# Optimization experiments

Measured on AMD Instinct MI355X. Metric: run time of the kernel, lower is better.

Reference implementation:

```python
import jax, jax.numpy as jnp
import numpy as np

S_LEN, T_LEN, BATCH, HID = 32, 32, 64, 512


def setup_inputs() -> dict:
    key = jax.random.key(0)
    ks = jax.random.split(key, 5)
    H = HID
    sc = lambda n: 1.0 / np.sqrt(n)
    return {
        "source": jax.random.normal(ks[0], (S_LEN, BATCH, H), jnp.float32),
        "target": jax.random.normal(ks[1], (T_LEN, BATCH, H), jnp.float32),
        # H2h Dense: concat(s_h, t_h) [B, 2H] -> [B, H], linear
        "W_H2h": (jax.random.normal(ks[2], (2 * H, H), jnp.float32) * sc(2 * H)),
        "b_H2h": jnp.zeros((H,), jnp.float32),
        # shared LSTMCell weights (Keras gate order i, f, g, o)
        "W_kernel": (jax.random.normal(ks[3], (H, 4 * H), jnp.float32) * sc(H)),
        "W_rec": (jax.random.normal(ks[4], (H, 4 * H), jnp.float32) * sc(H)),
        "b_lstm": jnp.zeros((4 * H,), jnp.float32),
    }


def _lstm_cell(x, h, c, Wk, Wr, b):
    # Keras LSTMCell math, gate order i, f, g(candidate), o
    z = x @ Wk + h @ Wr + b  # [B, 4H]
    i, f, g, o = jnp.split(z, 4, axis=-1)
    c2 = jax.nn.sigmoid(f) * c + jax.nn.sigmoid(i) * jnp.tanh(g)
    h2 = jax.nn.sigmoid(o) * jnp.tanh(c2)
    return h2, c2


def reference(source, target, W_H2h, b_H2h, W_kernel, W_rec, b_lstm):
    # source: [S, B, H] (time-major), target: [T, B, H]
    T, B, H = target.shape

    def inner(s_state, t_slice):
        # s_state carried along the target axis; t_slice is target cell j state
        s_step, s_h, s_m = s_state
        t_step, t_h, t_m = t_slice
        hmid = jnp.concatenate([s_h, t_h], axis=1) @ W_H2h + b_H2h  # [B, H]
        ns_h, ns_m = _lstm_cell(s_step, hmid, s_m, W_kernel, W_rec, b_lstm)
        nt_h, nt_m = _lstm_cell(t_step, hmid, t_m, W_kernel, W_rec, b_lstm)
        # step arrays get overwritten with the new hidden state
        return (ns_h, ns_h, ns_m), (nt_h, nt_h, nt_m)

    def outer(t_arrays, s_in):
        # fresh source state per outer step i: step = source[i], h = m = 0
        z = jnp.zeros_like(s_in)
        (s_step_f, _, _), t_new = jax.lax.scan(inner, (s_in, z, z), t_arrays)
        return t_new, s_step_f

    zeros = jnp.zeros((T, B, H), source.dtype)
    t_final, source_out = jax.lax.scan(outer, (target, zeros, zeros), source)
    return source_out, t_final[0]
```

## Files before the change

### kernel.cpp

```cpp
#include <hip/hip_runtime.h>

#define BLK 256

typedef __bf16 bf16;
typedef __bf16 bf16x8 __attribute__((ext_vector_type(8)));
typedef float f32x4 __attribute__((ext_vector_type(4)));

__device__ __forceinline__ float sigm(float x) { return 1.f / (1.f + __expf(-x)); }
__device__ __forceinline__ float tanh_(float x) {
    x = fminf(fmaxf(x, -15.f), 15.f);
    float e = __expf(2.f * x);
    return (e - 1.f) / (e + 1.f);
}

__device__ __forceinline__ void gl2lds(const bf16* g, bf16* l) {
    __builtin_amdgcn_global_load_lds((const __attribute__((address_space(1))) void*)g,
                                     (__attribute__((address_space(3))) void*)l, 16, 0, 0);
}


__global__ void k_cast(const float* __restrict__ in, bf16* __restrict__ out, int n) {
    int i = blockIdx.x * BLK + threadIdx.x;
    if (i < n) out[i] = (bf16)in[i];
}

__global__ void k_cast2(const float* __restrict__ in, bf16* __restrict__ hi,
                        bf16* __restrict__ lo, int n) {
    int i = blockIdx.x * BLK + threadIdx.x;
    if (i < n) {
        float v = in[i];
        bf16 h = (bf16)v;
        hi[i] = h;
        lo[i] = (bf16)(v - (float)h);
    }
}

__global__ void k_tcast2(const float* __restrict__ in, bf16* __restrict__ hi,
                         bf16* __restrict__ lo, int C) {
    int id = blockIdx.x * BLK + threadIdx.x;
    int c = id >> 9, r = id & 511;
    float v = in[(size_t)r * C + c];
    bf16 h = (bf16)v;
    hi[id] = h;
    if (lo) lo[id] = (bf16)(v - (float)h);
}

__global__ void k_bz(const float* __restrict__ bh, const float* __restrict__ Wr,
                     const float* __restrict__ bl, float* __restrict__ bz) {
    int c = blockIdx.x * BLK + threadIdx.x;
    float s = bl[c];
    for (int k = 0; k < 512; k++) s += bh[k] * Wr[(size_t)k * 2048 + c];
    bz[c] = s;
}

__global__ __launch_bounds__(256, 2) void k_gemmP(
    const bf16* __restrict__ Ahi, const bf16* __restrict__ Alo,
    const bf16* __restrict__ Bhi, const bf16* __restrict__ Blo,
    const float* __restrict__ Wk,
    bf16* __restrict__ P1, bf16* __restrict__ P3,
    bf16* __restrict__ P4, bf16* __restrict__ P5) {
    __shared__ __align__(16) bf16 At[64 * 72];
    __shared__ __align__(16) bf16 Bt[4 * 64 * 72];
    const int t = threadIdx.x, w = t >> 6, l = t & 63;
    const int m0 = (blockIdx.x >> 2) * 64, n0 = (blockIdx.x & 3) * 256;
    f32x4 acc[4][4] = {};
    const bf16* Aps[3] = {Ahi, Alo, Ahi};
    const bf16* Bps[3] = {Bhi, Bhi, Blo};
    for (int p = 0; p < 3; p++) {
        const bf16* Ap = Aps[p] + (size_t)m0 * 512;
        const bf16* Bp = Bps[p];
        for (int kt = 0; kt < 8; kt++) {
            int k0 = kt * 64;
            __syncthreads();
#pragma unroll
            for (int q = 0; q < 2; q++) {
                int idx = q * 256 + t, row = idx >> 3, cc = idx & 7;
                uint4 v = *(const uint4*)(Ap + (size_t)row * 512 + k0 + cc * 8);
                *(uint4*)&At[row * 72 + cc * 8] = v;
            }
#pragma unroll
            for (int q = 0; q < 8; q++) {
                int idx = q * 256 + t, g = idx >> 9, rr = (idx >> 3) & 63, cc = idx & 7;
                uint4 v = *(const uint4*)(Bp + (size_t)(n0 + g * 64 + rr) * 512 + k0 + cc * 8);
                *(uint4*)&Bt[(g * 64 + rr) * 72 + cc * 8] = v;
            }
            __syncthreads();
#pragma unroll
            for (int ks = 0; ks < 2; ks++) {
                int ko = ks * 32 + (l >> 4) * 8;
                bf16x8 af[4], bb[4];
#pragma unroll
                for (int mt = 0; mt < 4; mt++)
                    af[mt] = *(const bf16x8*)&At[(mt * 16 + (l & 15)) * 72 + ko];
#pragma unroll
                for (int g = 0; g < 4; g++)
                    bb[g] = *(const bf16x8*)&Bt[(g * 64 + w * 16 + (l & 15)) * 72 + ko];
#pragma unroll
                for (int mt = 0; mt < 4; mt++)
#pragma unroll
                    for (int g = 0; g < 4; g++)
                        acc[mt][g] = __builtin_amdgcn_mfma_f32_16x16x32_bf16(
                            af[mt], bb[g], acc[mt][g], 0, 0, 0);
            }
        }
    }
    const bool hihalf = (n0 >= 512);
#pragma unroll
    for (int mt = 0; mt < 4; mt++) {
#pragma unroll
        for (int g = 0; g < 4; g++) {
            int np = n0 + g * 64 + w * 16 + (l & 15);
#pragma unroll
            for (int r = 0; r < 4; r++) {
                int c = m0 + mt * 16 + ((l >> 4) << 2) + r;
                float v = acc[mt][g][r];
                if (!hihalf) {
                    P4[(size_t)c * 512 + np] = (bf16)v;
                    P1[(size_t)c * 512 + np] = (bf16)(v + Wk[(size_t)np * 2048 + c]);
                } else {
                    int kk = np - 512;
                    P3[(size_t)c * 512 + kk] = (bf16)v;
                    P5[(size_t)c * 512 + kk] = (bf16)(v + Wk[(size_t)kk * 2048 + c]);
                }
            }
        }
    }
}

__global__ __launch_bounds__(256, 4) void k_diag(
    int d, int i_lo,
    const bf16* __restrict__ srcb, const bf16* __restrict__ tgtb,
    const bf16* __restrict__ P1, const bf16* __restrict__ P2,
    const bf16* __restrict__ P3, const bf16* __restrict__ P4,
    const bf16* __restrict__ P5,
    const float* __restrict__ bz,
    const bf16* __restrict__ shR, bf16* __restrict__ shW,
    const bf16* __restrict__ thR, bf16* __restrict__ thW,
    float* __restrict__ sc, float* __restrict__ tc,
    float* __restrict__ out) {
    __shared__ __align__(16) bf16 At[64 * 64];
    __shared__ __align__(16) bf16 Bt[128 * 64];
    const int t = threadIdx.x, w = t >> 6, l = t & 63;
    const int cell = blockIdx.x >> 5, sub = blockIdx.x & 31;
    const int side = sub >> 4, ch0 = (sub & 15) << 5;
    const int i = i_lo + cell, j = d - i;
    const size_t stI = (size_t)i * 64 * 512, stJ = (size_t)j * 64 * 512;

    const bf16* Ah[2];
    const bf16* Wh[2];
    int nh = 0;
    if (side == 0) {
        Ah[nh] = (j == 0 ? srcb : shR) + stI;
        Wh[nh] = (j == 0 ? P2 : P1);
        nh++;
        if (i > 0) { Ah[nh] = thR + stJ; Wh[nh] = P3; nh++; }
    } else {
        if (j > 0) { Ah[nh] = shR + stI; Wh[nh] = P4; nh++; }
        Ah[nh] = (i == 0 ? tgtb : thR) + stJ;
        Wh[nh] = (i == 0 ? P2 : P5);
        nh++;
    }

    f32x4 acc[2][4] = {};
    for (int hh = 0; hh < nh; hh++) {
        const bf16* Ap = Ah[hh];
        const bf16* Wp = Wh[hh];
        for (int kt = 0; kt < 8; kt++) {
            int k0 = kt * 64;
            __syncthreads();
#pragma unroll
            for (int q = 0; q < 2; q++) {
                int p = q * 256 + t;
                int r = p >> 3, c = (p & 7) ^ (r & 7);
                gl2lds(Ap + (size_t)r * 512 + k0 + c * 8, &At[(q * 256 + w * 64) * 8]);
            }
#pragma unroll
            for (int q = 0; q < 4; q++) {
                int p = q * 256 + t;
                int r = p >> 3, c = (p & 7) ^ (r & 7);
                int g = r >> 5;
                gl2lds(Wp + (size_t)(g * 512 + ch0 + (r & 31)) * 512 + k0 + c * 8,
                       &Bt[(q * 256 + w * 64) * 8]);
            }
            __syncthreads();
#pragma unroll
            for (int ks = 0; ks < 2; ks++) {
                int c = ks * 4 + (l >> 4);
                bf16x8 af[2], bb[4];
#pragma unroll
                for (int mt = 0; mt < 2; mt++) {
                    int r = (w >> 1) * 32 + mt * 16 + (l & 15);
                    af[mt] = *(const bf16x8*)&At[(r * 8 + (c ^ (r & 7))) * 8];
                }
#pragma unroll
                for (int g = 0; g < 4; g++) {
                    int r = g * 32 + (w & 1) * 16 + (l & 15);
                    bb[g] = *(const bf16x8*)&Bt[(r * 8 + (c ^ (r & 7))) * 8];
                }
#pragma unroll
                for (int mt = 0; mt < 2; mt++)
#pragma unroll
                    for (int g = 0; g < 4; g++)
                        acc[mt][g] = __builtin_amdgcn_mfma_f32_16x16x32_bf16(
                            af[mt], bb[g], acc[mt][g], 0, 0, 0);
            }
        }
    }

    const int h = ch0 + (w & 1) * 16 + (l & 15);
    float bzv[4];
#pragma unroll
    for (int g = 0; g < 4; g++) bzv[g] = bz[g * 512 + h];
#pragma unroll
    for (int mt = 0; mt < 2; mt++) {
#pragma unroll
        for (int r = 0; r < 4; r++) {
            int b = (w >> 1) * 32 + mt * 16 + ((l >> 4) << 2) + r;
            float zi = acc[mt][0][r] + bzv[0];
            float zf = acc[mt][1][r] + bzv[1];
            float zg = acc[mt][2][r] + bzv[2];
            float zo = acc[mt][3][r] + bzv[3];
            if (side == 0) {
                size_t off = stI + (size_t)b * 512 + h;
                float cold = (j == 0) ? 0.f : sc[off];
                float c2 = sigm(zf) * cold + sigm(zi) * tanh_(zg);
                float h2 = sigm(zo) * tanh_(c2);
                sc[off] = c2;
                shW[off] = (bf16)h2;
                if (j == 31) out[off] = h2;
            } else {
                size_t off = stJ + (size_t)b * 512 + h;
                float cold = (i == 0) ? 0.f : tc[off];
                float c2 = sigm(zf) * cold + sigm(zi) * tanh_(zg);
                float h2 = sigm(zo) * tanh_(c2);
                tc[off] = c2;
                thW[off] = (bf16)h2;
                if (i == 31) out[1048576 + off] = h2;
            }
        }
    }
}


extern "C" void kernel_launch(void* const* d_in, const int* in_sizes, int n_in,
                              void* d_out, int out_size, void* d_ws, size_t ws_size,
                              hipStream_t stream) {
    const float* src = (const float*)d_in[0];
    const float* tgt = (const float*)d_in[1];
    const float* WH = (const float*)d_in[2];
    const float* bH = (const float*)d_in[3];
    const float* Wk = (const float*)d_in[4];
    const float* Wr = (const float*)d_in[5];
    const float* bl = (const float*)d_in[6];
    float* out = (float*)d_out;
    char* w = (char*)d_ws;
    const size_t MB = 1u << 20;
    bf16* srcb = (bf16*)(w + 0 * MB);
    bf16* tgtb = (bf16*)(w + 2 * MB);
    bf16* WHhi = (bf16*)(w + 4 * MB);
    bf16* WHlo = (bf16*)(w + 5 * MB);
    bf16* Wrhi = (bf16*)(w + 6 * MB);
    bf16* Wrlo = (bf16*)(w + 8 * MB);
    bf16* P1 = (bf16*)(w + 10 * MB);
    bf16* P2 = (bf16*)(w + 12 * MB);
    bf16* P3 = (bf16*)(w + 14 * MB);
    bf16* P4 = (bf16*)(w + 16 * MB);
    bf16* P5 = (bf16*)(w + 18 * MB);
    float* bz = (float*)(w + 20 * MB);
    bf16* sh = (bf16*)(w + 21 * MB);
    bf16* th = (bf16*)(w + 25 * MB);
    float* sc = (float*)(w + 29 * MB);
    float* tc = (float*)(w + 33 * MB);

    k_cast<<<4096, BLK, 0, stream>>>(src, srcb, 1048576);
    k_cast<<<4096, BLK, 0, stream>>>(tgt, tgtb, 1048576);
    k_cast2<<<2048, BLK, 0, stream>>>(WH, WHhi, WHlo, 524288);
    k_tcast2<<<4096, BLK, 0, stream>>>(Wr, Wrhi, Wrlo, 2048);
    k_tcast2<<<4096, BLK, 0, stream>>>(Wk, P2, nullptr, 2048);
    k_bz<<<8, BLK, 0, stream>>>(bH, Wr, bl, bz);
    k_gemmP<<<128, BLK, 0, stream>>>(Wrhi, Wrlo, WHhi, WHlo, Wk, P1, P3, P4, P5);

    for (int d = 0; d < 63; d++) {
        int i_lo = d > 31 ? d - 31 : 0;
        int i_hi = d < 31 ? d : 31;
        int Kd = i_hi - i_lo + 1;
        const bf16* shR = sh + (size_t)(d & 1) * 1048576;
        bf16* shW = sh + (size_t)((d + 1) & 1) * 1048576;
        const bf16* thR = th + (size_t)(d & 1) * 1048576;
        bf16* thW = th + (size_t)((d + 1) & 1) * 1048576;
        k_diag<<<Kd * 32, BLK, 0, stream>>>(d, i_lo, srcb, tgtb, P1, P2, P3, P4, P5,
                                            bz, shR, shW, thR, thW, sc, tc, out);
    }
}
```

Before: 1.467 ms.

## Replace per-diagonal launches with persistent wavefront kernel using per-cell dependency counters

Replaces the 63 per-diagonal kernel launches with a single persistent cooperative kernel. Blocks walk the tiles diagonal by diagonal and spin on per-cell completion counters in global memory before starting a cell. The five prep kernels are merged into one grid-stride kernel, which also zeroes the counters. The A operand is now read straight into registers with relaxed atomic loads instead of through LDS, each wave covers 16 rows and all 128 gate columns, and hidden states are written as packed pairs. This removes launch overhead and the full-grid barrier at each diagonal, at the cost of spin-wait latency and relaxed-ordering memory-visibility risks.

```diff
diff --git a/kernel.cpp b/kernel.cpp
--- a/kernel.cpp
+++ b/kernel.cpp
@@ -5,6 +5,7 @@
 typedef __bf16 bf16;
 typedef __bf16 bf16x8 __attribute__((ext_vector_type(8)));
 typedef float f32x4 __attribute__((ext_vector_type(4)));
+typedef unsigned long long u64;
 
 __device__ __forceinline__ float sigm(float x) { return 1.f / (1.f + __expf(-x)); }
 __device__ __forceinline__ float tanh_(float x) {
@@ -18,39 +19,47 @@
                                      (__attribute__((address_space(3))) void*)l, 16, 0, 0);
 }
 
-
-__global__ void k_cast(const float* __restrict__ in, bf16* __restrict__ out, int n) {
-    int i = blockIdx.x * BLK + threadIdx.x;
-    if (i < n) out[i] = (bf16)in[i];
-}
-
-__global__ void k_cast2(const float* __restrict__ in, bf16* __restrict__ hi,
-                        bf16* __restrict__ lo, int n) {
-    int i = blockIdx.x * BLK + threadIdx.x;
-    if (i < n) {
-        float v = in[i];
+#define ALOAD64(p) __hip_atomic_load((const u64*)(p), __ATOMIC_RELAXED, __HIP_MEMORY_SCOPE_AGENT)
+#define ALOADF(p) __hip_atomic_load((const float*)(p), __ATOMIC_RELAXED, __HIP_MEMORY_SCOPE_AGENT)
+#define ASTOREF(p, v) __hip_atomic_store((float*)(p), (v), __ATOMIC_RELAXED, __HIP_MEMORY_SCOPE_AGENT)
+#define ASTOREU(p, v) __hip_atomic_store((unsigned int*)(p), (v), __ATOMIC_RELAXED, __HIP_MEMORY_SCOPE_AGENT)
+
+__global__ void k_prep(const float* __restrict__ src, const float* __restrict__ tgt,
+                       const float* __restrict__ WH, const float* __restrict__ bH,
+                       const float* __restrict__ Wk, const float* __restrict__ Wr,
+                       const float* __restrict__ bl,
+                       bf16* __restrict__ srcb, bf16* __restrict__ tgtb,
+                       bf16* __restrict__ WHhi, bf16* __restrict__ WHlo,
+                       bf16* __restrict__ Wrhi, bf16* __restrict__ Wrlo,
+                       bf16* __restrict__ P2, float* __restrict__ bz,
+                       int* __restrict__ cellDone) {
+    const int gtid = blockIdx.x * BLK + threadIdx.x;
+    const int NT = gridDim.x * BLK;
+    for (int id = gtid; id < 1048576; id += NT) srcb[id] = (bf16)src[id];
+    for (int id = gtid; id < 1048576; id += NT) tgtb[id] = (bf16)tgt[id];
+    for (int id = gtid; id < 524288; id += NT) {
+        float v = WH[id];
         bf16 h = (bf16)v;
-        hi[i] = h;
-        lo[i] = (bf16)(v - (float)h);
-    }
-}
-
-__global__ void k_tcast2(const float* __restrict__ in, bf16* __restrict__ hi,
-                         bf16* __restrict__ lo, int C) {
-    int id = blockIdx.x * BLK + threadIdx.x;
-    int c = id >> 9, r = id & 511;
-    float v = in[(size_t)r * C + c];
-    bf16 h = (bf16)v;
-    hi[id] = h;
-    if (lo) lo[id] = (bf16)(v - (float)h);
-}
-
-__global__ void k_bz(const float* __restrict__ bh, const float* __restrict__ Wr,
-                     const float* __restrict__ bl, float* __restrict__ bz) {
-    int c = blockIdx.x * BLK + threadIdx.x;
-    float s = bl[c];
-    for (int k = 0; k < 512; k++) s += bh[k] * Wr[(size_t)k * 2048 + c];
-    bz[c] = s;
+        WHhi[id] = h;
+        WHlo[id] = (bf16)(v - (float)h);
+    }
+    for (int id = gtid; id < 1048576; id += NT) {
+        int c = id >> 9, r = id & 511;
+        float v = Wr[(size_t)r * 2048 + c];
+        bf16 h = (bf16)v;
+        Wrhi[id] = h;
+        Wrlo[id] = (bf16)(v - (float)h);
+    }
+    for (int id = gtid; id < 1048576; id += NT) {
+        int c = id >> 9, r = id & 511;
+        P2[id] = (bf16)Wk[(size_t)r * 2048 + c];
+    }
+    for (int id = gtid; id < 2048; id += NT) {
+        float s = bl[id];
+        for (int k = 0; k < 512; k++) s += bH[k] * Wr[(size_t)k * 2048 + id];
+        bz[id] = s;
+    }
+    for (int id = gtid; id < 1024; id += NT) cellDone[id] = 0;
 }
 
 __global__ __launch_bounds__(256, 2) void k_gemmP(
@@ -127,117 +136,161 @@
     }
 }
 
-__global__ __launch_bounds__(256, 4) void k_diag(
-    int d, int i_lo,
-    const bf16* __restrict__ srcb, const bf16* __restrict__ tgtb,
-    const bf16* __restrict__ P1, const bf16* __restrict__ P2,
-    const bf16* __restrict__ P3, const bf16* __restrict__ P4,
-    const bf16* __restrict__ P5,
-    const float* __restrict__ bz,
-    const bf16* __restrict__ shR, bf16* __restrict__ shW,
-    const bf16* __restrict__ thR, bf16* __restrict__ thW,
-    float* __restrict__ sc, float* __restrict__ tc,
-    float* __restrict__ out) {
-    __shared__ __align__(16) bf16 At[64 * 64];
+struct WaveP {
+    const bf16 *srcb, *tgtb, *P1, *P2, *P3, *P4, *P5;
+    const float* bz;
+    bf16 *sh, *th;
+    float *sc, *tc;
+    float* out;
+    int* cellDone;
+    int nblk;
+};
+
+__global__ __launch_bounds__(256, 4) void k_wave(WaveP p) {
     __shared__ __align__(16) bf16 Bt[128 * 64];
     const int t = threadIdx.x, w = t >> 6, l = t & 63;
-    const int cell = blockIdx.x >> 5, sub = blockIdx.x & 31;
-    const int side = sub >> 4, ch0 = (sub & 15) << 5;
-    const int i = i_lo + cell, j = d - i;
-    const size_t stI = (size_t)i * 64 * 512, stJ = (size_t)j * 64 * 512;
-
-    const bf16* Ah[2];
-    const bf16* Wh[2];
-    int nh = 0;
-    if (side == 0) {
-        Ah[nh] = (j == 0 ? srcb : shR) + stI;
-        Wh[nh] = (j == 0 ? P2 : P1);
-        nh++;
-        if (i > 0) { Ah[nh] = thR + stJ; Wh[nh] = P3; nh++; }
-    } else {
-        if (j > 0) { Ah[nh] = shR + stI; Wh[nh] = P4; nh++; }
-        Ah[nh] = (i == 0 ? tgtb : thR) + stJ;
-        Wh[nh] = (i == 0 ? P2 : P5);
-        nh++;
-    }
-
-    f32x4 acc[2][4] = {};
-    for (int hh = 0; hh < nh; hh++) {
-        const bf16* Ap = Ah[hh];
-        const bf16* Wp = Wh[hh];
-        for (int kt = 0; kt < 8; kt++) {
-            int k0 = kt * 64;
+    const int bid = blockIdx.x;
+    const int nblk = p.nblk;
+
+    int J = bid, base = 0;
+#pragma unroll 1
+    for (int d = 0; d < 63; d++) {
+        const int i_lo = d > 31 ? d - 31 : 0;
+        const int Kd = d < 32 ? d + 1 : 63 - d;
+        const int cnt = Kd * 32;
+#pragma unroll 1
+        while (J - base < cnt) {
+            const int tile = J - base;
+            const int cell = tile >> 5, sub = tile & 31;
+            const int side = sub >> 4, ch0 = (sub & 15) << 5;
+            const int i = i_lo + cell, j = d - i;
+            const size_t stI = (size_t)i * 64 * 512, stJ = (size_t)j * 64 * 512;
+
+            if (t == 0) {
+                if (j > 0)
+                    while (__hip_atomic_load(&p.cellDone[i * 32 + j - 1], __ATOMIC_RELAXED,
+                                             __HIP_MEMORY_SCOPE_AGENT) < 32)
+                        __builtin_amdgcn_s_sleep(4);
+                if (i > 0)
+                    while (__hip_atomic_load(&p.cellDone[(i - 1) * 32 + j], __ATOMIC_RELAXED,
+                                             __HIP_MEMORY_SCOPE_AGENT) < 32)
+                        __builtin_amdgcn_s_sleep(4);
+            }
             __syncthreads();
-#pragma unroll
-            for (int q = 0; q < 2; q++) {
-                int p = q * 256 + t;
-                int r = p >> 3, c = (p & 7) ^ (r & 7);
-                gl2lds(Ap + (size_t)r * 512 + k0 + c * 8, &At[(q * 256 + w * 64) * 8]);
-            }
-#pragma unroll
-            for (int q = 0; q < 4; q++) {
-                int p = q * 256 + t;
-                int r = p >> 3, c = (p & 7) ^ (r & 7);
-                int g = r >> 5;
-                gl2lds(Wp + (size_t)(g * 512 + ch0 + (r & 31)) * 512 + k0 + c * 8,
-                       &Bt[(q * 256 + w * 64) * 8]);
-            }
+
+            const bf16* shR = p.sh + (size_t)(d & 1) * 1048576;
+            bf16* shW = p.sh + (size_t)((d + 1) & 1) * 1048576;
+            const bf16* thR = p.th + (size_t)(d & 1) * 1048576;
+            bf16* thW = p.th + (size_t)((d + 1) & 1) * 1048576;
+
+            const bf16* Ah[2];
+            const bf16* Wh[2];
+            int nh = 0;
+            if (side == 0) {
+                Ah[nh] = (j == 0 ? p.srcb : shR) + stI;
+                Wh[nh] = (j == 0 ? p.P2 : p.P1);
+                nh++;
+                if (i > 0) { Ah[nh] = thR + stJ; Wh[nh] = p.P3; nh++; }
+            } else {
+                if (j > 0) { Ah[nh] = shR + stI; Wh[nh] = p.P4; nh++; }
+                Ah[nh] = (i == 0 ? p.tgtb : thR) + stJ;
+                Wh[nh] = (i == 0 ? p.P2 : p.P5);
+                nh++;
+            }
+
+            f32x4 acc[8] = {};
+            for (int hh = 0; hh < nh; hh++) {
+                const bf16* Ap = Ah[hh];
+                const bf16* Wp = Wh[hh];
+                for (int kt = 0; kt < 8; kt++) {
+                    int k0 = kt * 64;
+                    __syncthreads();
+#pragma unroll
+                    for (int q = 0; q < 4; q++) {
+                        int pp = q * 256 + t;
+                        int r = pp >> 3, c = (pp & 7) ^ (r & 7);
+                        int g = r >> 5;
+                        gl2lds(Wp + (size_t)(g * 512 + ch0 + (r & 31)) * 512 + k0 + c * 8,
+                               &Bt[(q * 256 + w * 64) * 8]);
+                    }
+                    u64 areg[2][2];
+                    {
+                        const int r = w * 16 + (l & 15);
+                        const u64* Ap64 = (const u64*)Ap + (size_t)r * 128;
+#pragma unroll
+                        for (int ks = 0; ks < 2; ks++) {
+                            int ko = k0 + ks * 32 + (l >> 4) * 8;
+                            areg[ks][0] = ALOAD64(Ap64 + (ko >> 2));
+                            areg[ks][1] = ALOAD64(Ap64 + (ko >> 2) + 1);
+                        }
+                    }
+                    __syncthreads();
+#pragma unroll
+                    for (int ks = 0; ks < 2; ks++) {
+                        int c = ks * 4 + (l >> 4);
+                        union { u64 u[2]; bf16x8 v; } cv;
+                        cv.u[0] = areg[ks][0];
+                        cv.u[1] = areg[ks][1];
+                        bf16x8 af = cv.v;
+#pragma unroll
+                        for (int g8 = 0; g8 < 8; g8++) {
+                            int r = g8 * 16 + (l & 15);
+                            bf16x8 bb = *(const bf16x8*)&Bt[(r * 8 + (c ^ (r & 7))) * 8];
+                            acc[g8] = __builtin_amdgcn_mfma_f32_16x16x32_bf16(af, bb, acc[g8], 0, 0, 0);
+                        }
+                    }
+                }
+            }
+
+            union { bf16 b; unsigned short s; } c0, c1;
+#pragma unroll
+            for (int hh16 = 0; hh16 < 2; hh16++) {
+                const int h = ch0 + hh16 * 16 + (l & 15);
+                float bzv[4];
+#pragma unroll
+                for (int g = 0; g < 4; g++) bzv[g] = p.bz[g * 512 + h];
+#pragma unroll
+                for (int r = 0; r < 4; r++) {
+                    int b = w * 16 + ((l >> 4) << 2) + r;
+                    float zi = acc[0 * 2 + hh16][r] + bzv[0];
+                    float zf = acc[1 * 2 + hh16][r] + bzv[1];
+                    float zg = acc[2 * 2 + hh16][r] + bzv[2];
+                    float zo = acc[3 * 2 + hh16][r] + bzv[3];
+                    size_t off = (side == 0 ? stI : stJ) + (size_t)b * 512 + h;
+                    float cold;
+                    if (side == 0)
+                        cold = (j == 0) ? 0.f : ALOADF(&p.sc[off]);
+                    else
+                        cold = (i == 0) ? 0.f : ALOADF(&p.tc[off]);
+                    float c2 = sigm(zf) * cold + sigm(zi) * tanh_(zg);
+                    float h2 = sigm(zo) * tanh_(c2);
+                    if (side == 0)
+                        ASTOREF(&p.sc[off], c2);
+                    else
+                        ASTOREF(&p.tc[off], c2);
+                    float hp = __shfl_xor(h2, 1);
+                    c0.b = (bf16)h2;
+                    c1.b = (bf16)hp;
+                    unsigned int packed = (unsigned int)c0.s | ((unsigned int)c1.s << 16);
+                    if (!(l & 1)) {
+                        bf16* hw = (side == 0 ? shW : thW);
+                        ASTOREU(&hw[off], packed);
+                    }
+                    if (side == 0) {
+                        if (j == 31) p.out[off] = h2;
+                    } else if (i == 31) {
+                        p.out[1048576 + off] = h2;
+                    }
+                }
+            }
+
             __syncthreads();
-#pragma unroll
-            for (int ks = 0; ks < 2; ks++) {
-                int c = ks * 4 + (l >> 4);
-                bf16x8 af[2], bb[4];
-#pragma unroll
-                for (int mt = 0; mt < 2; mt++) {
-                    int r = (w >> 1) * 32 + mt * 16 + (l & 15);
-                    af[mt] = *(const bf16x8*)&At[(r * 8 + (c ^ (r & 7))) * 8];
-                }
-#pragma unroll
-                for (int g = 0; g < 4; g++) {
-                    int r = g * 32 + (w & 1) * 16 + (l & 15);
-                    bb[g] = *(const bf16x8*)&Bt[(r * 8 + (c ^ (r & 7))) * 8];
-                }
-#pragma unroll
-                for (int mt = 0; mt < 2; mt++)
-#pragma unroll
-                    for (int g = 0; g < 4; g++)
-                        acc[mt][g] = __builtin_amdgcn_mfma_f32_16x16x32_bf16(
-                            af[mt], bb[g], acc[mt][g], 0, 0, 0);
-            }
+            if (t == 0)
+                __hip_atomic_fetch_add(&p.cellDone[i * 32 + j], 1, __ATOMIC_RELAXED,
+                                       __HIP_MEMORY_SCOPE_AGENT);
+            J += nblk;
         }
-    }
-
-    const int h = ch0 + (w & 1) * 16 + (l & 15);
-    float bzv[4];
-#pragma unroll
-    for (int g = 0; g < 4; g++) bzv[g] = bz[g * 512 + h];
-#pragma unroll
-    for (int mt = 0; mt < 2; mt++) {
-#pragma unroll
-        for (int r = 0; r < 4; r++) {
-            int b = (w >> 1) * 32 + mt * 16 + ((l >> 4) << 2) + r;
-            float zi = acc[mt][0][r] + bzv[0];
-            float zf = acc[mt][1][r] + bzv[1];
-            float zg = acc[mt][2][r] + bzv[2];
-            float zo = acc[mt][3][r] + bzv[3];
-            if (side == 0) {
-                size_t off = stI + (size_t)b * 512 + h;
-                float cold = (j == 0) ? 0.f : sc[off];
-                float c2 = sigm(zf) * cold + sigm(zi) * tanh_(zg);
-                float h2 = sigm(zo) * tanh_(c2);
-                sc[off] = c2;
-                shW[off] = (bf16)h2;
-                if (j == 31) out[off] = h2;
-            } else {
-                size_t off = stJ + (size_t)b * 512 + h;
-                float cold = (i == 0) ? 0.f : tc[off];
-                float c2 = sigm(zf) * cold + sigm(zi) * tanh_(zg);
-                float h2 = sigm(zo) * tanh_(c2);
-                tc[off] = c2;
-                thW[off] = (bf16)h2;
-                if (i == 31) out[1048576 + off] = h2;
-            }
-        }
+        base += cnt;
     }
 }
 
@@ -245,6 +298,8 @@
 extern "C" void kernel_launch(void* const* d_in, const int* in_sizes, int n_in,
                               void* d_out, int out_size, void* d_ws, size_t ws_size,
                               hipStream_t stream) {
+    char* w = (char*)d_ws;
+    const size_t MB = 1u << 20;
     const float* src = (const float*)d_in[0];
     const float* tgt = (const float*)d_in[1];
     const float* WH = (const float*)d_in[2];
@@ -252,9 +307,7 @@
     const float* Wk = (const float*)d_in[4];
     const float* Wr = (const float*)d_in[5];
     const float* bl = (const float*)d_in[6];
-    float* out = (float*)d_out;
-    char* w = (char*)d_ws;
-    const size_t MB = 1u << 20;
+
     bf16* srcb = (bf16*)(w + 0 * MB);
     bf16* tgtb = (bf16*)(w + 2 * MB);
     bf16* WHhi = (bf16*)(w + 4 * MB);
@@ -271,24 +324,34 @@
     bf16* th = (bf16*)(w + 25 * MB);
     float* sc = (float*)(w + 29 * MB);
     float* tc = (float*)(w + 33 * MB);
-
-    k_cast<<<4096, BLK, 0, stream>>>(src, srcb, 1048576);
-    k_cast<<<4096, BLK, 0, stream>>>(tgt, tgtb, 1048576);
-    k_cast2<<<2048, BLK, 0, stream>>>(WH, WHhi, WHlo, 524288);
-    k_tcast2<<<4096, BLK, 0, stream>>>(Wr, Wrhi, Wrlo, 2048);
-    k_tcast2<<<4096, BLK, 0, stream>>>(Wk, P2, nullptr, 2048);
-    k_bz<<<8, BLK, 0, stream>>>(bH, Wr, bl, bz);
+    int* cellDone = (int*)(w + 37 * MB);
+
+    k_prep<<<2048, BLK, 0, stream>>>(src, tgt, WH, bH, Wk, Wr, bl, srcb, tgtb,
+                                     WHhi, WHlo, Wrhi, Wrlo, P2, bz, cellDone);
     k_gemmP<<<128, BLK, 0, stream>>>(Wrhi, Wrlo, WHhi, WHlo, Wk, P1, P3, P4, P5);
 
-    for (int d = 0; d < 63; d++) {
-        int i_lo = d > 31 ? d - 31 : 0;
-        int i_hi = d < 31 ? d : 31;
-        int Kd = i_hi - i_lo + 1;
-        const bf16* shR = sh + (size_t)(d & 1) * 1048576;
-        bf16* shW = sh + (size_t)((d + 1) & 1) * 1048576;
-        const bf16* thR = th + (size_t)(d & 1) * 1048576;
-        bf16* thW = th + (size_t)((d + 1) & 1) * 1048576;
-        k_diag<<<Kd * 32, BLK, 0, stream>>>(d, i_lo, srcb, tgtb, P1, P2, P3, P4, P5,
-                                            bz, shR, shW, thR, thW, sc, tc, out);
-    }
-}
+    WaveP p;
+    p.srcb = srcb; p.tgtb = tgtb;
+    p.P1 = P1; p.P2 = P2; p.P3 = P3; p.P4 = P4; p.P5 = P5;
+    p.bz = bz; p.sh = sh; p.th = th; p.sc = sc; p.tc = tc;
+    p.out = (float*)d_out;
+    p.cellDone = cellDone;
+
+    int dev = 0;
+    hipGetDevice(&dev);
+    int numCU = 0;
+    hipDeviceGetAttribute(&numCU, hipDeviceAttributeMultiprocessorCount, dev);
+    int occ = 0;
+    hipOccupancyMaxActiveBlocksPerMultiprocessor(&occ, (const void*)k_wave, BLK, 0);
+    int nblk = occ * numCU;
+    if (nblk > 1024) nblk = 1024;
+    if (nblk < 1) nblk = 1;
+    p.nblk = nblk;
+
+    void* args[] = {&p};
+    hipError_t err =
+        hipLaunchCooperativeKernel((void*)k_wave, dim3(nblk), dim3(BLK), args, 0, stream);
+    if (err != hipSuccess) {
+        k_wave<<<nblk, BLK, 0, stream>>>(p);
+    }
+}
```

New measurement: 2.570 ms. 75.1% more time.

## Pair diagonal cells per block to share weight tiles, fuse prep kernels

Applied to the files above, without the earlier changes.

Each diagonal-step block now processes two adjacent cells that use the same weight panels. It stages a 4x larger weight tile in LDS once and feeds both cells' MFMAs from it, with activations read directly from global memory. This halves grid size per diagonal and cuts redundant weight loads, at the cost of fewer blocks (less parallelism on short diagonals) and more registers (launch bound 2). The six preprocessing kernels are merged into one prep kernel with a tiled LDS transpose, and the precompute GEMM is retiled to smaller blocks with swizzled direct-to-LDS loads.

```diff
diff --git a/kernel.cpp b/kernel.cpp
--- a/kernel.cpp
+++ b/kernel.cpp
@@ -18,85 +18,104 @@
                                      (__attribute__((address_space(3))) void*)l, 16, 0, 0);
 }
 
-
-__global__ void k_cast(const float* __restrict__ in, bf16* __restrict__ out, int n) {
-    int i = blockIdx.x * BLK + threadIdx.x;
-    if (i < n) out[i] = (bf16)in[i];
-}
-
-__global__ void k_cast2(const float* __restrict__ in, bf16* __restrict__ hi,
-                        bf16* __restrict__ lo, int n) {
-    int i = blockIdx.x * BLK + threadIdx.x;
-    if (i < n) {
-        float v = in[i];
-        bf16 h = (bf16)v;
-        hi[i] = h;
-        lo[i] = (bf16)(v - (float)h);
-    }
-}
-
-__global__ void k_tcast2(const float* __restrict__ in, bf16* __restrict__ hi,
-                         bf16* __restrict__ lo, int C) {
-    int id = blockIdx.x * BLK + threadIdx.x;
-    int c = id >> 9, r = id & 511;
-    float v = in[(size_t)r * C + c];
-    bf16 h = (bf16)v;
-    hi[id] = h;
-    if (lo) lo[id] = (bf16)(v - (float)h);
-}
-
-__global__ void k_bz(const float* __restrict__ bh, const float* __restrict__ Wr,
-                     const float* __restrict__ bl, float* __restrict__ bz) {
-    int c = blockIdx.x * BLK + threadIdx.x;
-    float s = bl[c];
-    for (int k = 0; k < 512; k++) s += bh[k] * Wr[(size_t)k * 2048 + c];
-    bz[c] = s;
-}
-
-__global__ __launch_bounds__(256, 2) void k_gemmP(
-    const bf16* __restrict__ Ahi, const bf16* __restrict__ Alo,
-    const bf16* __restrict__ Bhi, const bf16* __restrict__ Blo,
+__global__ __launch_bounds__(256) void k_prep(
+    const float* __restrict__ src, const float* __restrict__ tgt,
+    const float* __restrict__ WH, const float* __restrict__ bH,
+    const float* __restrict__ Wk, const float* __restrict__ Wr,
+    const float* __restrict__ bl,
+    bf16* __restrict__ srcb, bf16* __restrict__ tgtb,
+    bf16* __restrict__ WHhi, bf16* __restrict__ WHlo,
+    bf16* __restrict__ Wrhi, bf16* __restrict__ Wrlo,
+    bf16* __restrict__ P2, float* __restrict__ bz) {
+    __shared__ float tile[64][65];
+    const int bid = blockIdx.x, t = threadIdx.x;
+    if (bid < 512) {
+        const float* in = (bid < 256) ? Wr : Wk;
+        bf16* ohi = (bid < 256) ? Wrhi : P2;
+        bf16* olo = (bid < 256) ? Wrlo : nullptr;
+        const int b = bid & 255;
+        const int tr = b >> 5, tc = b & 31;
+#pragma unroll
+        for (int q = 0; q < 16; q++) {
+            int idx = q * 256 + t, lr = idx >> 6, lc = idx & 63;
+            tile[lr][lc] = in[(size_t)(tr * 64 + lr) * 2048 + tc * 64 + lc];
+        }
+        __syncthreads();
+#pragma unroll
+        for (int q = 0; q < 16; q++) {
+            int idx = q * 256 + t, lr = idx >> 6, lc = idx & 63;
+            float v = tile[lc][lr];
+            size_t o = (size_t)(tc * 64 + lr) * 512 + tr * 64 + lc;
+            bf16 h = (bf16)v;
+            ohi[o] = h;
+            if (olo) olo[o] = (bf16)(v - (float)h);
+        }
+    } else if (bid < 520) {
+        int c = (bid - 512) * 256 + t;
+        float s = bl[c];
+        for (int k = 0; k < 512; k++) s += bH[k] * Wr[(size_t)k * 2048 + c];
+        bz[c] = s;
+    } else {
+        const int gt = (bid - 520) * 256 + t, NT = 504 * 256;
+        for (int id = gt; id < 1048576; id += NT) srcb[id] = (bf16)src[id];
+        for (int id = gt; id < 1048576; id += NT) tgtb[id] = (bf16)tgt[id];
+        for (int id = gt; id < 524288; id += NT) {
+            float v = WH[id];
+            bf16 h = (bf16)v;
+            WHhi[id] = h;
+            WHlo[id] = (bf16)(v - (float)h);
+        }
+    }
+}
+
+__global__ __launch_bounds__(256, 4) void k_gemmP(
+    const bf16* __restrict__ Wrhi, const bf16* __restrict__ Wrlo,
+    const bf16* __restrict__ WHhi, const bf16* __restrict__ WHlo,
     const float* __restrict__ Wk,
     bf16* __restrict__ P1, bf16* __restrict__ P3,
     bf16* __restrict__ P4, bf16* __restrict__ P5) {
-    __shared__ __align__(16) bf16 At[64 * 72];
-    __shared__ __align__(16) bf16 Bt[4 * 64 * 72];
+    __shared__ __align__(16) bf16 At[64 * 64];
+    __shared__ __align__(16) bf16 Bt[128 * 64];
     const int t = threadIdx.x, w = t >> 6, l = t & 63;
-    const int m0 = (blockIdx.x >> 2) * 64, n0 = (blockIdx.x & 3) * 256;
-    f32x4 acc[4][4] = {};
-    const bf16* Aps[3] = {Ahi, Alo, Ahi};
-    const bf16* Bps[3] = {Bhi, Bhi, Blo};
-    for (int p = 0; p < 3; p++) {
-        const bf16* Ap = Aps[p] + (size_t)m0 * 512;
-        const bf16* Bp = Bps[p];
+    const int m0 = (blockIdx.x >> 3) * 64, n0 = (blockIdx.x & 7) * 128;
+    f32x4 acc[2][4] = {};
+    const bf16* Aps[3] = {Wrhi, Wrlo, Wrhi};
+    const bf16* Bps[3] = {WHhi, WHhi, WHlo};
+    for (int ph = 0; ph < 3; ph++) {
+        const bf16* Ap = Aps[ph] + (size_t)m0 * 512;
+        const bf16* Bp = Bps[ph] + (size_t)n0 * 512;
         for (int kt = 0; kt < 8; kt++) {
             int k0 = kt * 64;
             __syncthreads();
 #pragma unroll
             for (int q = 0; q < 2; q++) {
-                int idx = q * 256 + t, row = idx >> 3, cc = idx & 7;
-                uint4 v = *(const uint4*)(Ap + (size_t)row * 512 + k0 + cc * 8);
-                *(uint4*)&At[row * 72 + cc * 8] = v;
-            }
-#pragma unroll
-            for (int q = 0; q < 8; q++) {
-                int idx = q * 256 + t, g = idx >> 9, rr = (idx >> 3) & 63, cc = idx & 7;
-                uint4 v = *(const uint4*)(Bp + (size_t)(n0 + g * 64 + rr) * 512 + k0 + cc * 8);
-                *(uint4*)&Bt[(g * 64 + rr) * 72 + cc * 8] = v;
+                int pp = q * 256 + t;
+                int r = pp >> 3, c = (pp & 7) ^ (r & 7);
+                gl2lds(Ap + (size_t)r * 512 + k0 + c * 8, &At[(q * 256 + w * 64) * 8]);
+            }
+#pragma unroll
+            for (int q = 0; q < 4; q++) {
+                int pp = q * 256 + t;
+                int r = pp >> 3, c = (pp & 7) ^ (r & 7);
+                gl2lds(Bp + (size_t)r * 512 + k0 + c * 8, &Bt[(q * 256 + w * 64) * 8]);
             }
             __syncthreads();
 #pragma unroll
             for (int ks = 0; ks < 2; ks++) {
-                int ko = ks * 32 + (l >> 4) * 8;
-                bf16x8 af[4], bb[4];
-#pragma unroll
-                for (int mt = 0; mt < 4; mt++)
-                    af[mt] = *(const bf16x8*)&At[(mt * 16 + (l & 15)) * 72 + ko];
-#pragma unroll
-                for (int g = 0; g < 4; g++)
-                    bb[g] = *(const bf16x8*)&Bt[(g * 64 + w * 16 + (l & 15)) * 72 + ko];
-#pragma unroll
-                for (int mt = 0; mt < 4; mt++)
+                int c = ks * 4 + (l >> 4);
+                bf16x8 af[2], bb[4];
+#pragma unroll
+                for (int mt = 0; mt < 2; mt++) {
+                    int r = (w >> 1) * 32 + mt * 16 + (l & 15);
+                    af[mt] = *(const bf16x8*)&At[(r * 8 + (c ^ (r & 7))) * 8];
+                }
+#pragma unroll
+                for (int g = 0; g < 4; g++) {
+                    int r = g * 32 + (w & 1) * 16 + (l & 15);
+                    bb[g] = *(const bf16x8*)&Bt[(r * 8 + (c ^ (r & 7))) * 8];
+                }
+#pragma unroll
+                for (int mt = 0; mt < 2; mt++)
 #pragma unroll
                     for (int g = 0; g < 4; g++)
                         acc[mt][g] = __builtin_amdgcn_mfma_f32_16x16x32_bf16(
@@ -106,13 +125,13 @@
     }
     const bool hihalf = (n0 >= 512);
 #pragma unroll
-    for (int mt = 0; mt < 4; mt++) {
+    for (int mt = 0; mt < 2; mt++) {
 #pragma unroll
         for (int g = 0; g < 4; g++) {
-            int np = n0 + g * 64 + w * 16 + (l & 15);
+            int np = n0 + g * 32 + (w & 1) * 16 + (l & 15);
 #pragma unroll
             for (int r = 0; r < 4; r++) {
-                int c = m0 + mt * 16 + ((l >> 4) << 2) + r;
+                int c = m0 + (w >> 1) * 32 + mt * 16 + ((l >> 4) << 2) + r;
                 float v = acc[mt][g][r];
                 if (!hihalf) {
                     P4[(size_t)c * 512 + np] = (bf16)v;
@@ -127,8 +146,86 @@
     }
 }
 
-__global__ __launch_bounds__(256, 4) void k_diag(
-    int d, int i_lo,
+__device__ __forceinline__ void do_phase(const bf16* __restrict__ A0,
+                                         const bf16* __restrict__ A1,
+                                         const bf16* __restrict__ Wp, int ch0, int t,
+                                         int w, int l, bf16* Bt, f32x4 (*acc0)[4],
+                                         f32x4 (*acc1)[4]) {
+#pragma unroll 1
+    for (int ktg = 0; ktg < 2; ktg++) {
+        __syncthreads();
+#pragma unroll
+        for (int q = 0; q < 4; q++) {
+            int k0 = (ktg * 4 + q) * 64;
+#pragma unroll
+            for (int io = 0; io < 4; io++) {
+                int pp = io * 256 + t;
+                int r = pp >> 3, c = (pp & 7) ^ (r & 7), g = r >> 5;
+                gl2lds(Wp + (size_t)(g * 512 + ch0 + (r & 31)) * 512 + k0 + c * 8,
+                       &Bt[(q * 1024 + io * 256 + w * 64) * 8]);
+            }
+        }
+        __syncthreads();
+#pragma unroll
+        for (int q = 0; q < 4; q++) {
+            int k0 = (ktg * 4 + q) * 64;
+            bf16x8 a0[2][2], a1[2][2];
+#pragma unroll
+            for (int ks = 0; ks < 2; ks++)
+#pragma unroll
+                for (int mt = 0; mt < 2; mt++) {
+                    int r = (w >> 1) * 32 + mt * 16 + (l & 15);
+                    size_t off = (size_t)r * 512 + k0 + ks * 32 + (l >> 4) * 8;
+                    a0[ks][mt] = *(const bf16x8*)(A0 + off);
+                    if (A1) a1[ks][mt] = *(const bf16x8*)(A1 + off);
+                }
+#pragma unroll
+            for (int ks = 0; ks < 2; ks++) {
+                int cq = ks * 4 + (l >> 4);
+#pragma unroll
+                for (int g = 0; g < 4; g++) {
+                    int r = g * 32 + (w & 1) * 16 + (l & 15);
+                    bf16x8 bb = *(const bf16x8*)&Bt[(q * 1024 + r * 8 + (cq ^ (r & 7))) * 8];
+#pragma unroll
+                    for (int mt = 0; mt < 2; mt++) {
+                        acc0[mt][g] = __builtin_amdgcn_mfma_f32_16x16x32_bf16(
+                            a0[ks][mt], bb, acc0[mt][g], 0, 0, 0);
+                        if (A1)
+                            acc1[mt][g] = __builtin_amdgcn_mfma_f32_16x16x32_bf16(
+                                a1[ks][mt], bb, acc1[mt][g], 0, 0, 0);
+                    }
+                }
+            }
+        }
+    }
+}
+
+__device__ __forceinline__ int build_panels(int i, int d, int side,
+                                            const bf16* srcb, const bf16* tgtb,
+                                            const bf16* shR, const bf16* thR,
+                                            const bf16* P1, const bf16* P2,
+                                            const bf16* P3, const bf16* P4,
+                                            const bf16* P5, const bf16** A,
+                                            const bf16** W) {
+    const int j = d - i;
+    const size_t stI = (size_t)i * 32768, stJ = (size_t)j * 32768;
+    int nh = 0;
+    if (side == 0) {
+        A[nh] = (j == 0 ? srcb : shR) + stI;
+        W[nh] = (j == 0 ? P2 : P1);
+        nh++;
+        if (i > 0) { A[nh] = thR + stJ; W[nh] = P3; nh++; }
+    } else {
+        if (j > 0) { A[nh] = shR + stI; W[nh] = P4; nh++; }
+        A[nh] = (i == 0 ? tgtb : thR) + stJ;
+        W[nh] = (i == 0 ? P2 : P5);
+        nh++;
+    }
+    return nh;
+}
+
+__global__ __launch_bounds__(256, 2) void k_diag2(
+    int d, int i_lo, int i_hi,
     const bf16* __restrict__ srcb, const bf16* __restrict__ tgtb,
     const bf16* __restrict__ P1, const bf16* __restrict__ P2,
     const bf16* __restrict__ P3, const bf16* __restrict__ P4,
@@ -138,104 +235,67 @@
     const bf16* __restrict__ thR, bf16* __restrict__ thW,
     float* __restrict__ sc, float* __restrict__ tc,
     float* __restrict__ out) {
-    __shared__ __align__(16) bf16 At[64 * 64];
-    __shared__ __align__(16) bf16 Bt[128 * 64];
+    __shared__ __align__(16) bf16 Bt[4 * 128 * 64];
     const int t = threadIdx.x, w = t >> 6, l = t & 63;
-    const int cell = blockIdx.x >> 5, sub = blockIdx.x & 31;
+    const int pairI = blockIdx.x >> 5, sub = blockIdx.x & 31;
     const int side = sub >> 4, ch0 = (sub & 15) << 5;
-    const int i = i_lo + cell, j = d - i;
-    const size_t stI = (size_t)i * 64 * 512, stJ = (size_t)j * 64 * 512;
-
-    const bf16* Ah[2];
-    const bf16* Wh[2];
-    int nh = 0;
-    if (side == 0) {
-        Ah[nh] = (j == 0 ? srcb : shR) + stI;
-        Wh[nh] = (j == 0 ? P2 : P1);
-        nh++;
-        if (i > 0) { Ah[nh] = thR + stJ; Wh[nh] = P3; nh++; }
+    const int ia = i_lo + pairI * 2;
+    const int ib = ia + 1;
+    const bool v1 = (ib <= i_hi);
+
+    const bf16 *A0[2], *W0[2], *A1[2], *W1[2];
+    const int nh0 = build_panels(ia, d, side, srcb, tgtb, shR, thR, P1, P2, P3, P4, P5, A0, W0);
+    int nh1 = 0;
+    if (v1) nh1 = build_panels(ib, d, side, srcb, tgtb, shR, thR, P1, P2, P3, P4, P5, A1, W1);
+    const bool share = v1 && (nh0 == nh1) && (W0[0] == W1[0]) && (nh0 < 2 || W0[1] == W1[1]);
+
+    f32x4 acc0[2][4] = {}, acc1[2][4] = {};
+    if (share) {
+        for (int hh = 0; hh < nh0; hh++)
+            do_phase(A0[hh], A1[hh], W0[hh], ch0, t, w, l, Bt, acc0, acc1);
     } else {
-        if (j > 0) { Ah[nh] = shR + stI; Wh[nh] = P4; nh++; }
-        Ah[nh] = (i == 0 ? tgtb : thR) + stJ;
-        Wh[nh] = (i == 0 ? P2 : P5);
-        nh++;
-    }
-
-    f32x4 acc[2][4] = {};
-    for (int hh = 0; hh < nh; hh++) {
-        const bf16* Ap = Ah[hh];
-        const bf16* Wp = Wh[hh];
-        for (int kt = 0; kt < 8; kt++) {
-            int k0 = kt * 64;
-            __syncthreads();
-#pragma unroll
-            for (int q = 0; q < 2; q++) {
-                int p = q * 256 + t;
-                int r = p >> 3, c = (p & 7) ^ (r & 7);
-                gl2lds(Ap + (size_t)r * 512 + k0 + c * 8, &At[(q * 256 + w * 64) * 8]);
-            }
-#pragma unroll
-            for (int q = 0; q < 4; q++) {
-                int p = q * 256 + t;
-                int r = p >> 3, c = (p & 7) ^ (r & 7);
-                int g = r >> 5;
-                gl2lds(Wp + (size_t)(g * 512 + ch0 + (r & 31)) * 512 + k0 + c * 8,
-                       &Bt[(q * 256 + w * 64) * 8]);
-            }
-            __syncthreads();
-#pragma unroll
-            for (int ks = 0; ks < 2; ks++) {
-                int c = ks * 4 + (l >> 4);
-                bf16x8 af[2], bb[4];
-#pragma unroll
-                for (int mt = 0; mt < 2; mt++) {
-                    int r = (w >> 1) * 32 + mt * 16 + (l & 15);
-                    af[mt] = *(const bf16x8*)&At[(r * 8 + (c ^ (r & 7))) * 8];
-                }
-#pragma unroll
-                for (int g = 0; g < 4; g++) {
-                    int r = g * 32 + (w & 1) * 16 + (l & 15);
-                    bb[g] = *(const bf16x8*)&Bt[(r * 8 + (c ^ (r & 7))) * 8];
-                }
-#pragma unroll
-                for (int mt = 0; mt < 2; mt++)
-#pragma unroll
-                    for (int g = 0; g < 4; g++)
-                        acc[mt][g] = __builtin_amdgcn_mfma_f32_16x16x32_bf16(
-                            af[mt], bb[g], acc[mt][g], 0, 0, 0);
-            }
-        }
+        for (int hh = 0; hh < nh0; hh++)
+            do_phase(A0[hh], nullptr, W0[hh], ch0, t, w, l, Bt, acc0, acc0);
+        if (v1)
+            for (int hh = 0; hh < nh1; hh++)
+                do_phase(A1[hh], nullptr, W1[hh], ch0, t, w, l, Bt, acc1, acc1);
     }
 
     const int h = ch0 + (w & 1) * 16 + (l & 15);
     float bzv[4];
 #pragma unroll
     for (int g = 0; g < 4; g++) bzv[g] = bz[g * 512 + h];
-#pragma unroll
-    for (int mt = 0; mt < 2; mt++) {
-#pragma unroll
-        for (int r = 0; r < 4; r++) {
-            int b = (w >> 1) * 32 + mt * 16 + ((l >> 4) << 2) + r;
-            float zi = acc[mt][0][r] + bzv[0];
-            float zf = acc[mt][1][r] + bzv[1];
-            float zg = acc[mt][2][r] + bzv[2];
-            float zo = acc[mt][3][r] + bzv[3];
-            if (side == 0) {
-                size_t off = stI + (size_t)b * 512 + h;
-                float cold = (j == 0) ? 0.f : sc[off];
-                float c2 = sigm(zf) * cold + sigm(zi) * tanh_(zg);
-                float h2 = sigm(zo) * tanh_(c2);
-                sc[off] = c2;
-                shW[off] = (bf16)h2;
-                if (j == 31) out[off] = h2;
-            } else {
-                size_t off = stJ + (size_t)b * 512 + h;
-                float cold = (i == 0) ? 0.f : tc[off];
-                float c2 = sigm(zf) * cold + sigm(zi) * tanh_(zg);
-                float h2 = sigm(zo) * tanh_(c2);
-                tc[off] = c2;
-                thW[off] = (bf16)h2;
-                if (i == 31) out[1048576 + off] = h2;
+    const int ncell = v1 ? 2 : 1;
+    for (int s = 0; s < ncell; s++) {
+        const int i = ia + s, j = d - i;
+        const size_t stI = (size_t)i * 32768, stJ = (size_t)j * 32768;
+        f32x4(*acc)[4] = s ? acc1 : acc0;
+#pragma unroll
+        for (int mt = 0; mt < 2; mt++) {
+#pragma unroll
+            for (int r = 0; r < 4; r++) {
+                int b = (w >> 1) * 32 + mt * 16 + ((l >> 4) << 2) + r;
+                float zi = acc[mt][0][r] + bzv[0];
+                float zf = acc[mt][1][r] + bzv[1];
+                float zg = acc[mt][2][r] + bzv[2];
+                float zo = acc[mt][3][r] + bzv[3];
+                if (side == 0) {
+                    size_t off = stI + (size_t)b * 512 + h;
+                    float cold = (j == 0) ? 0.f : sc[off];
+                    float c2 = sigm(zf) * cold + sigm(zi) * tanh_(zg);
+                    float h2 = sigm(zo) * tanh_(c2);
+                    sc[off] = c2;
+                    shW[off] = (bf16)h2;
+                    if (j == 31) out[off] = h2;
+                } else {
+                    size_t off = stJ + (size_t)b * 512 + h;
+                    float cold = (i == 0) ? 0.f : tc[off];
+                    float c2 = sigm(zf) * cold + sigm(zi) * tanh_(zg);
+                    float h2 = sigm(zo) * tanh_(c2);
+                    tc[off] = c2;
+                    thW[off] = (bf16)h2;
+                    if (i == 31) out[1048576 + off] = h2;
+                }
             }
         }
     }
@@ -245,6 +305,8 @@
 extern "C" void kernel_launch(void* const* d_in, const int* in_sizes, int n_in,
                               void* d_out, int out_size, void* d_ws, size_t ws_size,
                               hipStream_t stream) {
+    char* w = (char*)d_ws;
+    const size_t MB = 1u << 20;
     const float* src = (const float*)d_in[0];
     const float* tgt = (const float*)d_in[1];
     const float* WH = (const float*)d_in[2];
@@ -253,8 +315,7 @@
     const float* Wr = (const float*)d_in[5];
     const float* bl = (const float*)d_in[6];
     float* out = (float*)d_out;
-    char* w = (char*)d_ws;
-    const size_t MB = 1u << 20;
+
     bf16* srcb = (bf16*)(w + 0 * MB);
     bf16* tgtb = (bf16*)(w + 2 * MB);
     bf16* WHhi = (bf16*)(w + 4 * MB);
@@ -272,23 +333,21 @@
     float* sc = (float*)(w + 29 * MB);
     float* tc = (float*)(w + 33 * MB);
 
-    k_cast<<<4096, BLK, 0, stream>>>(src, srcb, 1048576);
-    k_cast<<<4096, BLK, 0, stream>>>(tgt, tgtb, 1048576);
-    k_cast2<<<2048, BLK, 0, stream>>>(WH, WHhi, WHlo, 524288);
-    k_tcast2<<<4096, BLK, 0, stream>>>(Wr, Wrhi, Wrlo, 2048);
-    k_tcast2<<<4096, BLK, 0, stream>>>(Wk, P2, nullptr, 2048);
-    k_bz<<<8, BLK, 0, stream>>>(bH, Wr, bl, bz);
-    k_gemmP<<<128, BLK, 0, stream>>>(Wrhi, Wrlo, WHhi, WHlo, Wk, P1, P3, P4, P5);
+    k_prep<<<1024, BLK, 0, stream>>>(src, tgt, WH, bH, Wk, Wr, bl, srcb, tgtb,
+                                     WHhi, WHlo, Wrhi, Wrlo, P2, bz);
+    k_gemmP<<<256, BLK, 0, stream>>>(Wrhi, Wrlo, WHhi, WHlo, Wk, P1, P3, P4, P5);
 
     for (int d = 0; d < 63; d++) {
         int i_lo = d > 31 ? d - 31 : 0;
         int i_hi = d < 31 ? d : 31;
         int Kd = i_hi - i_lo + 1;
+        int nPair = (Kd + 1) >> 1;
         const bf16* shR = sh + (size_t)(d & 1) * 1048576;
         bf16* shW = sh + (size_t)((d + 1) & 1) * 1048576;
         const bf16* thR = th + (size_t)(d & 1) * 1048576;
         bf16* thW = th + (size_t)((d + 1) & 1) * 1048576;
-        k_diag<<<Kd * 32, BLK, 0, stream>>>(d, i_lo, srcb, tgtb, P1, P2, P3, P4, P5,
-                                            bz, shR, shW, thR, thW, sc, tc, out);
-    }
-}
+        k_diag2<<<nPair * 32, BLK, 0, stream>>>(d, i_lo, i_hi, srcb, tgtb, P1, P2, P3,
+                                                P4, P5, bz, shR, shW, thR, thW, sc, tc,
+                                                out);
+    }
+}
```

Measured after the change: 2.513 ms. 71.2% more time.
